# Performance work log

Hardware: AMD Instinct MI355X
Metric: run time of the kernel (lower is better)

## Reference

```python
import jax, jax.numpy as jnp
import numpy as np

NUM_EMBEDDINGS = 8192
EMBEDDING_DIM = 256


def setup_inputs() -> dict:
    key = jax.random.key(0)
    k1, k2 = jax.random.split(key)
    z = jax.random.normal(k1, (16, EMBEDDING_DIM, 32, 32), dtype=jnp.float32)
    # nn.Embedding default init: N(0, 1)
    emb_table = jax.random.normal(k2, (NUM_EMBEDDINGS, EMBEDDING_DIM), dtype=jnp.float32)
    return {"z": z, "emb_table": emb_table}


def reference(z, emb_table):
    # z: [B, D, H, W]; emb_table: [K, D]
    B, D, H, W = z.shape
    # flatten to per-token vectors: [B*H*W, D]
    zf = z.reshape(B, D, H * W).transpose(0, 2, 1).reshape(B * H * W, D)
    Wt = jax.lax.stop_gradient(emb_table)  # original detaches W for distance
    # argmin of mean squared distance == argmin of squared distance;
    # expand ||z - w||^2 = ||z||^2 - 2 z.w + ||w||^2 (avoid (N,K,D) expansion)
    z_sq = jnp.sum(zf * zf, axis=-1, keepdims=True)          # [N, 1]
    w_sq = jnp.sum(Wt * Wt, axis=-1)                          # [K]
    dists = z_sq - 2.0 * (zf @ Wt.T) + w_sq                   # [N, K]
    token_ids = jnp.argmin(dists, axis=-1)                    # [N]
    quantized = emb_table[token_ids]                          # [N, D] (differentiable gather)
    return quantized.reshape(B, H * W, D).transpose(0, 2, 1).reshape(B, D, H, W)
```

## Files before the change

### kernel.cpp

```cpp
#include <hip/hip_runtime.h>
#include <stdint.h>

#define DIM 256
#define NEMB 8192
#define NTOK 16384
#define HW 1024

typedef __attribute__((ext_vector_type(4))) int int4v;

__device__ __forceinline__ void async_cp16(void* lds, const void* g) {
  __builtin_amdgcn_global_load_lds(
      (const __attribute__((address_space(1))) unsigned int*)g,
      (__attribute__((address_space(3))) unsigned int*)lds, 16, 0, 0);
}
__device__ __forceinline__ int q0_of(float x) {
  int q = __float2int_rn(x * 20.0f);
  return q > 127 ? 127 : (q < -127 ? -127 : q);
}
__device__ __forceinline__ int q1_of(float x, int q0) {
  float e = x * 20.0f - (float)q0;
  int q = __float2int_rn(e * 128.0f);
  return q > 127 ? 127 : (q < -127 ? -127 : q);
}
__device__ __forceinline__ unsigned int pack4(int a, int b, int c, int d) {
  return (unsigned int)(a & 0xff) | ((unsigned int)(b & 0xff) << 8) |
         ((unsigned int)(c & 0xff) << 16) | ((unsigned int)(d & 0xff) << 24);
}

__global__ __launch_bounds__(256) void prep_w_kernel(
    const float* __restrict__ emb, unsigned int* __restrict__ q0w,
    unsigned int* __restrict__ q1w, int* __restrict__ iwsq2) {
  int lane = threadIdx.x & 63;
  int row = blockIdx.x * 4 + (threadIdx.x >> 6);
  const float4 v = *(const float4*)(emb + (size_t)row * DIM + lane * 4);
  float s = v.x * v.x + v.y * v.y + v.z * v.z + v.w * v.w;
  int a0 = q0_of(v.x), b0 = q0_of(v.y), c0 = q0_of(v.z), d0 = q0_of(v.w);
  q0w[row * (DIM / 4) + lane] = pack4(a0, b0, c0, d0);
  q1w[row * (DIM / 4) + lane] =
      pack4(q1_of(v.x, a0), q1_of(v.y, b0), q1_of(v.z, c0), q1_of(v.w, d0));
#pragma unroll
  for (int off = 32; off > 0; off >>= 1) s += __shfl_xor(s, off, 64);
  if (lane == 0) iwsq2[row] = (int)rintf(s * 25600.0f) + 8192;
}

__global__ __launch_bounds__(256) void prep_z_kernel(
    const float* __restrict__ z, unsigned int* __restrict__ q0z,
    unsigned int* __restrict__ q1z, float* __restrict__ zf32) {
  __shared__ float tile[64][65];
  int b = blockIdx.x, d0 = blockIdx.y * 64, hw0 = blockIdx.z * 64;
  int tid = threadIdx.x;
  int lane = tid & 63, grp = tid >> 6;
  const float* src = z + (size_t)b * DIM * HW + hw0 + lane;
#pragma unroll
  for (int i = 0; i < 16; i++) {
    int dl = grp + i * 4;
    tile[dl][lane] = src[(size_t)(d0 + dl) * HW];
  }
  __syncthreads();
  int dq = tid & 15;
#pragma unroll
  for (int p = 0; p < 4; p++) {
    int n = (tid >> 4) + p * 16;
    float x0 = tile[dq * 4 + 0][n], x1 = tile[dq * 4 + 1][n];
    float x2 = tile[dq * 4 + 2][n], x3 = tile[dq * 4 + 3][n];
    int a0 = q0_of(x0), b0 = q0_of(x1), c0 = q0_of(x2), e0 = q0_of(x3);
    int token = b * HW + hw0 + n;
    size_t off = (size_t)token * (DIM / 4) + (d0 >> 2) + dq;
    q0z[off] = pack4(a0, b0, c0, e0);
    q1z[off] = pack4(q1_of(x0, a0), q1_of(x1, b0), q1_of(x2, c0), q1_of(x3, e0));
    *(float4*)(zf32 + (size_t)token * DIM + d0 + dq * 4) =
        make_float4(x0, x1, x2, x3);
  }
}

__global__ __launch_bounds__(256, 4) void gemm_topk_kernel(
    const signed char* __restrict__ q0z, const signed char* __restrict__ q1z,
    const signed char* __restrict__ q0w, const signed char* __restrict__ q1w,
    const int* __restrict__ iwsq2, uint2* __restrict__ partials) {
  __shared__ __align__(16) signed char sB[2][4][32 * 128];

  const int bid = blockIdx.x;
  const int xcd = bid & 7;
  const int kq = xcd >> 1;
  const int tg = (bid >> 3) + ((xcd & 1) << 7);
  const int tid = threadIdx.x;
  const int lane = tid & 63, w = tid >> 6;
  const int c = lane & 15, quad = lane >> 4;
  const int n0 = tg * 64;
  const int k0g = kq * 2048;

  int4v af0[4], af1[4];
  {
    const size_t arow = (size_t)(n0 + w * 16 + c) * DIM;
#pragma unroll
    for (int s = 0; s < 4; s++) {
      af0[s] = *(const int4v*)(q0z + arow + s * 64 + quad * 16);
      af1[s] = *(const int4v*)(q1z + arow + s * 64 + quad * 16);
    }
  }

  const int srow = tid >> 3;
  const int scl = ((tid & 7) ^ (srow & 7)) * 16;
  const signed char* p0 = q0w + (size_t)(k0g + srow) * DIM + scl;
  const signed char* p1 = q1w + (size_t)(k0g + srow) * DIM + scl;
  async_cp16(&sB[0][0][tid * 16], p0);
  async_cp16(&sB[0][1][tid * 16], p0 + 128);
  async_cp16(&sB[0][2][tid * 16], p1);
  async_cp16(&sB[0][3][tid * 16], p1 + 128);
  p0 += 32 * DIM;
  p1 += 32 * DIM;
  __syncthreads();

  unsigned int m1[4], m2[4];
#pragma unroll
  for (int i = 0; i < 4; i++) { m1[i] = 0xFFFFFFFFu; m2[i] = 0xFFFFFFFFu; }

  unsigned int idx0 = (unsigned)(k0g + c);
  const int4v zero = {0, 0, 0, 0};

  for (int it = 0; it < 64; it++) {
    const int buf = it & 1;
    if (it + 1 < 64) {
      const int nb = buf ^ 1;
      async_cp16(&sB[nb][0][tid * 16], p0);
      async_cp16(&sB[nb][1][tid * 16], p0 + 128);
      async_cp16(&sB[nb][2][tid * 16], p1);
      async_cp16(&sB[nb][3][tid * 16], p1 + 128);
      p0 += 32 * DIM;
      p1 += 32 * DIM;
    }
    const int iw0 = iwsq2[k0g + it * 32 + c];
    const int iw1 = iwsq2[k0g + it * 32 + 16 + c];

    int4v b0a[4], b0b[4];
#pragma unroll
    for (int s = 0; s < 4; s++) {
      const int half = s >> 1;
      const int ph = ((((s & 1) << 2) + quad) ^ (c & 7)) * 16;
      b0a[s] = *(const int4v*)(&sB[buf][half][c * 128 + ph]);
      b0b[s] = *(const int4v*)(&sB[buf][half][(16 + c) * 128 + ph]);
    }
    int4v a0, a1;
    a0 = __builtin_amdgcn_mfma_i32_16x16x64_i8(af0[0], b0a[0], zero, 0, 0, 0);
    a1 = __builtin_amdgcn_mfma_i32_16x16x64_i8(af0[0], b0b[0], zero, 0, 0, 0);
#pragma unroll
    for (int s = 1; s < 4; s++) {
      a0 = __builtin_amdgcn_mfma_i32_16x16x64_i8(af0[s], b0a[s], a0, 0, 0, 0);
      a1 = __builtin_amdgcn_mfma_i32_16x16x64_i8(af0[s], b0b[s], a1, 0, 0, 0);
    }
#pragma unroll
    for (int r = 0; r < 4; r++) { a0[r] <<= 7; a1[r] <<= 7; }
#pragma unroll
    for (int s = 0; s < 4; s++) {
      a0 = __builtin_amdgcn_mfma_i32_16x16x64_i8(af1[s], b0a[s], a0, 0, 0, 0);
      a1 = __builtin_amdgcn_mfma_i32_16x16x64_i8(af1[s], b0b[s], a1, 0, 0, 0);
    }
#pragma unroll
    for (int s = 0; s < 4; s++) {
      const int half = s >> 1;
      const int ph = ((((s & 1) << 2) + quad) ^ (c & 7)) * 16;
      int4v t = *(const int4v*)(&sB[buf][2 + half][c * 128 + ph]);
      int4v u = *(const int4v*)(&sB[buf][2 + half][(16 + c) * 128 + ph]);
      a0 = __builtin_amdgcn_mfma_i32_16x16x64_i8(af0[s], t, a0, 0, 0, 0);
      a1 = __builtin_amdgcn_mfma_i32_16x16x64_i8(af0[s], u, a1, 0, 0, 0);
    }
#pragma unroll
    for (int r = 0; r < 4; r++) {
      unsigned int s0 = (unsigned int)(iw0 - a0[r]);
      unsigned int s1 = (unsigned int)(iw1 - a1[r]);
      s0 = s0 < 0x2000000u ? s0 : 0x1FFFFFFu;
      s1 = s1 < 0x2000000u ? s1 : 0x1FFFFFFu;
      unsigned int pk0 = ((s0 << 7) & 0xFFFFE000u) | idx0;
      unsigned int pk1 = ((s1 << 7) & 0xFFFFE000u) | (idx0 + 16);
      unsigned int v = pk0 < pk1 ? pk0 : pk1;
      unsigned int lo = v < m1[r] ? v : m1[r];
      unsigned int hi = v < m1[r] ? m1[r] : v;
      m2[r] = m2[r] < hi ? m2[r] : hi;
      m1[r] = lo;
    }
    idx0 += 32;
    __syncthreads();
  }

#pragma unroll
  for (int r = 0; r < 4; r++) {
    unsigned int a1m = m1[r], a2m = m2[r];
#pragma unroll
    for (int off = 1; off < 16; off <<= 1) {
      unsigned int o1 = __shfl_xor(a1m, off, 16);
      unsigned int o2 = __shfl_xor(a2m, off, 16);
      unsigned int n1 = a1m < o1 ? a1m : o1;
      unsigned int hi = a1m < o1 ? o1 : a1m;
      unsigned int l2 = a2m < o2 ? a2m : o2;
      a2m = hi < l2 ? hi : l2;
      a1m = n1;
    }
    m1[r] = a1m;
    m2[r] = a2m;
  }
  if (c == 0) {
#pragma unroll
    for (int r = 0; r < 4; r++) {
      int token = n0 + w * 16 + quad * 4 + r;
      partials[(size_t)kq * NTOK + token] = make_uint2(m1[r], m2[r]);
    }
  }
}

__global__ __launch_bounds__(256) void rescore_kernel(
    const uint2* __restrict__ partials, const float* __restrict__ zf32,
    const float* __restrict__ emb, int* __restrict__ ids) {
  int w = threadIdx.x >> 6, lane = threadIdx.x & 63;
  int token = blockIdx.x * 4 + w;
  unsigned int p[8];
#pragma unroll
  for (int q = 0; q < 4; q++) {
    uint2 t = partials[(size_t)q * NTOK + token];
    p[q * 2] = t.x;
    p[q * 2 + 1] = t.y;
  }
  unsigned int smin = p[0];
#pragma unroll
  for (int q = 1; q < 8; q++) smin = p[q] < smin ? p[q] : smin;
  const unsigned int thr = (smin >> 13) + 64;
  int ns = 0;
#pragma unroll
  for (int q = 0; q < 8; q++) ns += ((p[q] >> 13) <= thr) ? 1 : 0;
  if (ns == 1) {
    if (lane == 0) ids[token] = (int)(smin & 0x1FFFu);
    return;
  }
  const float4 zv = *(const float4*)(zf32 + (size_t)token * DIM + lane * 4);
  double best = 1e300;
  int bid = NEMB;
#pragma unroll
  for (int q = 0; q < 8; q++) {
    if ((p[q] >> 13) <= thr) {
      int id = (int)(p[q] & 0x1FFFu);
      const float4 wv = *(const float4*)(emb + (size_t)id * DIM + lane * 4);
      double s = (double)wv.x * ((double)wv.x - 2.0 * (double)zv.x) +
                 (double)wv.y * ((double)wv.y - 2.0 * (double)zv.y) +
                 (double)wv.z * ((double)wv.z - 2.0 * (double)zv.z) +
                 (double)wv.w * ((double)wv.w - 2.0 * (double)zv.w);
#pragma unroll
      for (int off = 32; off > 0; off >>= 1) s += __shfl_xor(s, off, 64);
      if (s < best || (s == best && id < bid)) {
        best = s;
        bid = id;
      }
    }
  }
  if (lane == 0) ids[token] = bid;
}

__global__ __launch_bounds__(256) void gather_kernel(
    const int* __restrict__ ids, const float* __restrict__ emb,
    float* __restrict__ out) {
  __shared__ float tile[32][257];
  __shared__ int sid[32];
  int b = blockIdx.x;
  int hw0 = blockIdx.y * 32;
  int tid = threadIdx.x;
  if (tid < 32) sid[tid] = ids[b * HW + hw0 + tid];
  __syncthreads();
  for (int i = 0; i < 32; i++)
    tile[i][tid] = emb[(size_t)sid[i] * DIM + tid];
  __syncthreads();
  int h = tid & 31, dg = tid >> 5;
  for (int i = 0; i < 32; i++) {
    int d = i * 8 + dg;
    out[(size_t)b * DIM * HW + (size_t)d * HW + hw0 + h] = tile[h][d];
  }
}

extern "C" void kernel_launch(void* const* d_in, const int* in_sizes, int n_in,
                              void* d_out, int out_size, void* d_ws, size_t ws_size,
                              hipStream_t stream) {
  const float* z = (const float*)d_in[0];
  const float* emb = (const float*)d_in[1];
  float* out = (float*)d_out;
  char* ws = (char*)d_ws;

  float* zf32 = (float*)d_out;

  signed char* q0w = (signed char*)(ws);
  signed char* q1w = (signed char*)(ws + 2097152);
  signed char* q0z = (signed char*)(ws + 4194304);
  signed char* q1z = (signed char*)(ws + 8388608);
  int* iwsq2 = (int*)(ws + 12582912);
  uint2* partials = (uint2*)(ws + 12615680);
  int* ids = (int*)(ws + 13139968);

  prep_w_kernel<<<dim3(2048), 256, 0, stream>>>(emb, (unsigned int*)q0w,
                                                (unsigned int*)q1w, iwsq2);
  prep_z_kernel<<<dim3(16, 4, 16), 256, 0, stream>>>(z, (unsigned int*)q0z,
                                                     (unsigned int*)q1z, zf32);
  gemm_topk_kernel<<<dim3(1024), 256, 0, stream>>>(q0z, q1z, q0w, q1w, iwsq2,
                                                   partials);
  rescore_kernel<<<dim3(4096), 256, 0, stream>>>(partials, zf32, emb, ids);
  gather_kernel<<<dim3(16, 32), 256, 0, stream>>>(ids, emb, out);
}
```

Measured before the change: 191.5 us.

## Merge prep kernels, retile GEMM to 64 tokens per wave, fuse rescore into gather

```diff
diff --git a/kernel.cpp b/kernel.cpp
--- a/kernel.cpp
+++ b/kernel.cpp
@@ -27,29 +27,30 @@
          ((unsigned int)(c & 0xff) << 16) | ((unsigned int)(d & 0xff) << 24);
 }
 
-__global__ __launch_bounds__(256) void prep_w_kernel(
+__global__ __launch_bounds__(256) void prep_kernel(
     const float* __restrict__ emb, unsigned int* __restrict__ q0w,
-    unsigned int* __restrict__ q1w, int* __restrict__ iwsq2) {
-  int lane = threadIdx.x & 63;
-  int row = blockIdx.x * 4 + (threadIdx.x >> 6);
-  const float4 v = *(const float4*)(emb + (size_t)row * DIM + lane * 4);
-  float s = v.x * v.x + v.y * v.y + v.z * v.z + v.w * v.w;
-  int a0 = q0_of(v.x), b0 = q0_of(v.y), c0 = q0_of(v.z), d0 = q0_of(v.w);
-  q0w[row * (DIM / 4) + lane] = pack4(a0, b0, c0, d0);
-  q1w[row * (DIM / 4) + lane] =
-      pack4(q1_of(v.x, a0), q1_of(v.y, b0), q1_of(v.z, c0), q1_of(v.w, d0));
-#pragma unroll
-  for (int off = 32; off > 0; off >>= 1) s += __shfl_xor(s, off, 64);
-  if (lane == 0) iwsq2[row] = (int)rintf(s * 25600.0f) + 8192;
-}
-
-__global__ __launch_bounds__(256) void prep_z_kernel(
+    unsigned int* __restrict__ q1w, int* __restrict__ iwsq2,
     const float* __restrict__ z, unsigned int* __restrict__ q0z,
-    unsigned int* __restrict__ q1z, float* __restrict__ zf32) {
+    unsigned int* __restrict__ q1z) {
   __shared__ float tile[64][65];
-  int b = blockIdx.x, d0 = blockIdx.y * 64, hw0 = blockIdx.z * 64;
   int tid = threadIdx.x;
-  int lane = tid & 63, grp = tid >> 6;
+  int lane = tid & 63;
+  if (blockIdx.x < 2048) {
+    int row = blockIdx.x * 4 + (tid >> 6);
+    const float4 v = *(const float4*)(emb + (size_t)row * DIM + lane * 4);
+    float s = v.x * v.x + v.y * v.y + v.z * v.z + v.w * v.w;
+    int a0 = q0_of(v.x), b0 = q0_of(v.y), c0 = q0_of(v.z), d0 = q0_of(v.w);
+    q0w[row * (DIM / 4) + lane] = pack4(a0, b0, c0, d0);
+    q1w[row * (DIM / 4) + lane] =
+        pack4(q1_of(v.x, a0), q1_of(v.y, b0), q1_of(v.z, c0), q1_of(v.w, d0));
+#pragma unroll
+    for (int off = 32; off > 0; off >>= 1) s += __shfl_xor(s, off, 64);
+    if (lane == 0) iwsq2[row] = (int)rintf(s * 25600.0f) + 8192;
+    return;
+  }
+  int idx = blockIdx.x - 2048;
+  int b = idx >> 6, d0 = ((idx >> 4) & 3) * 64, hw0 = (idx & 15) * 64;
+  int grp = tid >> 6;
   const float* src = z + (size_t)b * DIM * HW + hw0 + lane;
 #pragma unroll
   for (int i = 0; i < 16; i++) {
@@ -68,34 +69,32 @@
     size_t off = (size_t)token * (DIM / 4) + (d0 >> 2) + dq;
     q0z[off] = pack4(a0, b0, c0, e0);
     q1z[off] = pack4(q1_of(x0, a0), q1_of(x1, b0), q1_of(x2, c0), q1_of(x3, e0));
-    *(float4*)(zf32 + (size_t)token * DIM + d0 + dq * 4) =
-        make_float4(x0, x1, x2, x3);
-  }
-}
-
-__global__ __launch_bounds__(256, 4) void gemm_topk_kernel(
+  }
+}
+
+__global__ __launch_bounds__(128, 2) void gemm_topk_kernel(
     const signed char* __restrict__ q0z, const signed char* __restrict__ q1z,
     const signed char* __restrict__ q0w, const signed char* __restrict__ q1w,
     const int* __restrict__ iwsq2, uint2* __restrict__ partials) {
-  __shared__ __align__(16) signed char sB[2][4][32 * 128];
+  __shared__ __align__(16) signed char sB[2][4][16 * 128];
 
   const int bid = blockIdx.x;
-  const int xcd = bid & 7;
-  const int kq = xcd >> 1;
-  const int tg = (bid >> 3) + ((xcd & 1) << 7);
+  const int kq = bid & 7;
+  const int tg = bid >> 3;
   const int tid = threadIdx.x;
   const int lane = tid & 63, w = tid >> 6;
   const int c = lane & 15, quad = lane >> 4;
-  const int n0 = tg * 64;
-  const int k0g = kq * 2048;
-
-  int4v af0[4], af1[4];
-  {
-    const size_t arow = (size_t)(n0 + w * 16 + c) * DIM;
+  const int n0 = tg * 128;
+  const int k0g = kq * 1024;
+
+  int4v af0[4][4], af1[4][4];
+#pragma unroll
+  for (int t = 0; t < 4; t++) {
+    const size_t arow = (size_t)(n0 + w * 64 + t * 16 + c) * DIM;
 #pragma unroll
     for (int s = 0; s < 4; s++) {
-      af0[s] = *(const int4v*)(q0z + arow + s * 64 + quad * 16);
-      af1[s] = *(const int4v*)(q1z + arow + s * 64 + quad * 16);
+      af0[t][s] = *(const int4v*)(q0z + arow + s * 64 + quad * 16);
+      af1[t][s] = *(const int4v*)(q1z + arow + s * 64 + quad * 16);
     }
   }
 
@@ -107,13 +106,13 @@
   async_cp16(&sB[0][1][tid * 16], p0 + 128);
   async_cp16(&sB[0][2][tid * 16], p1);
   async_cp16(&sB[0][3][tid * 16], p1 + 128);
-  p0 += 32 * DIM;
-  p1 += 32 * DIM;
-  __syncthreads();
-
-  unsigned int m1[4], m2[4];
-#pragma unroll
-  for (int i = 0; i < 4; i++) { m1[i] = 0xFFFFFFFFu; m2[i] = 0xFFFFFFFFu; }
+  p0 += 16 * DIM;
+  p1 += 16 * DIM;
+  __syncthreads();
+
+  unsigned int m1[16], m2[16];
+#pragma unroll
+  for (int i = 0; i < 16; i++) { m1[i] = 0xFFFFFFFFu; m2[i] = 0xFFFFFFFFu; }
 
   unsigned int idx0 = (unsigned)(k0g + c);
   const int4v zero = {0, 0, 0, 0};
@@ -126,65 +125,63 @@
       async_cp16(&sB[nb][1][tid * 16], p0 + 128);
       async_cp16(&sB[nb][2][tid * 16], p1);
       async_cp16(&sB[nb][3][tid * 16], p1 + 128);
-      p0 += 32 * DIM;
-      p1 += 32 * DIM;
-    }
-    const int iw0 = iwsq2[k0g + it * 32 + c];
-    const int iw1 = iwsq2[k0g + it * 32 + 16 + c];
-
-    int4v b0a[4], b0b[4];
+      p0 += 16 * DIM;
+      p1 += 16 * DIM;
+    }
+    const int iw = iwsq2[k0g + it * 16 + c];
+
+    int4v b0[4];
 #pragma unroll
     for (int s = 0; s < 4; s++) {
-      const int half = s >> 1;
       const int ph = ((((s & 1) << 2) + quad) ^ (c & 7)) * 16;
-      b0a[s] = *(const int4v*)(&sB[buf][half][c * 128 + ph]);
-      b0b[s] = *(const int4v*)(&sB[buf][half][(16 + c) * 128 + ph]);
-    }
-    int4v a0, a1;
-    a0 = __builtin_amdgcn_mfma_i32_16x16x64_i8(af0[0], b0a[0], zero, 0, 0, 0);
-    a1 = __builtin_amdgcn_mfma_i32_16x16x64_i8(af0[0], b0b[0], zero, 0, 0, 0);
-#pragma unroll
-    for (int s = 1; s < 4; s++) {
-      a0 = __builtin_amdgcn_mfma_i32_16x16x64_i8(af0[s], b0a[s], a0, 0, 0, 0);
-      a1 = __builtin_amdgcn_mfma_i32_16x16x64_i8(af0[s], b0b[s], a1, 0, 0, 0);
-    }
-#pragma unroll
-    for (int r = 0; r < 4; r++) { a0[r] <<= 7; a1[r] <<= 7; }
+      b0[s] = *(const int4v*)(&sB[buf][s >> 1][c * 128 + ph]);
+    }
+    int4v a[4];
+#pragma unroll
+    for (int t = 0; t < 4; t++) {
+      a[t] = __builtin_amdgcn_mfma_i32_16x16x64_i8(af0[t][0], b0[0], zero, 0, 0, 0);
+#pragma unroll
+      for (int s = 1; s < 4; s++)
+        a[t] = __builtin_amdgcn_mfma_i32_16x16x64_i8(af0[t][s], b0[s], a[t], 0, 0, 0);
+    }
+#pragma unroll
+    for (int t = 0; t < 4; t++)
+#pragma unroll
+      for (int r = 0; r < 4; r++) a[t][r] <<= 7;
+#pragma unroll
+    for (int t = 0; t < 4; t++)
+#pragma unroll
+      for (int s = 0; s < 4; s++)
+        a[t] = __builtin_amdgcn_mfma_i32_16x16x64_i8(af1[t][s], b0[s], a[t], 0, 0, 0);
 #pragma unroll
     for (int s = 0; s < 4; s++) {
-      a0 = __builtin_amdgcn_mfma_i32_16x16x64_i8(af1[s], b0a[s], a0, 0, 0, 0);
-      a1 = __builtin_amdgcn_mfma_i32_16x16x64_i8(af1[s], b0b[s], a1, 0, 0, 0);
-    }
-#pragma unroll
-    for (int s = 0; s < 4; s++) {
-      const int half = s >> 1;
       const int ph = ((((s & 1) << 2) + quad) ^ (c & 7)) * 16;
-      int4v t = *(const int4v*)(&sB[buf][2 + half][c * 128 + ph]);
-      int4v u = *(const int4v*)(&sB[buf][2 + half][(16 + c) * 128 + ph]);
-      a0 = __builtin_amdgcn_mfma_i32_16x16x64_i8(af0[s], t, a0, 0, 0, 0);
-      a1 = __builtin_amdgcn_mfma_i32_16x16x64_i8(af0[s], u, a1, 0, 0, 0);
-    }
-#pragma unroll
-    for (int r = 0; r < 4; r++) {
-      unsigned int s0 = (unsigned int)(iw0 - a0[r]);
-      unsigned int s1 = (unsigned int)(iw1 - a1[r]);
-      s0 = s0 < 0x2000000u ? s0 : 0x1FFFFFFu;
-      s1 = s1 < 0x2000000u ? s1 : 0x1FFFFFFu;
-      unsigned int pk0 = ((s0 << 7) & 0xFFFFE000u) | idx0;
-      unsigned int pk1 = ((s1 << 7) & 0xFFFFE000u) | (idx0 + 16);
-      unsigned int v = pk0 < pk1 ? pk0 : pk1;
-      unsigned int lo = v < m1[r] ? v : m1[r];
-      unsigned int hi = v < m1[r] ? m1[r] : v;
-      m2[r] = m2[r] < hi ? m2[r] : hi;
-      m1[r] = lo;
-    }
-    idx0 += 32;
+      int4v b1 = *(const int4v*)(&sB[buf][2 + (s >> 1)][c * 128 + ph]);
+#pragma unroll
+      for (int t = 0; t < 4; t++)
+        a[t] = __builtin_amdgcn_mfma_i32_16x16x64_i8(af0[t][s], b1, a[t], 0, 0, 0);
+    }
+#pragma unroll
+    for (int t = 0; t < 4; t++) {
+#pragma unroll
+      for (int r = 0; r < 4; r++) {
+        unsigned int s0 = (unsigned int)(iw - a[t][r]);
+        s0 = s0 < 0x2000000u ? s0 : 0x1FFFFFFu;
+        unsigned int v = ((s0 << 7) & 0xFFFFE000u) | idx0;
+        const int ix = t * 4 + r;
+        unsigned int lo = v < m1[ix] ? v : m1[ix];
+        unsigned int hi = v < m1[ix] ? m1[ix] : v;
+        m2[ix] = m2[ix] < hi ? m2[ix] : hi;
+        m1[ix] = lo;
+      }
+    }
+    idx0 += 16;
     __syncthreads();
   }
 
 #pragma unroll
-  for (int r = 0; r < 4; r++) {
-    unsigned int a1m = m1[r], a2m = m2[r];
+  for (int ix = 0; ix < 16; ix++) {
+    unsigned int a1m = m1[ix], a2m = m2[ix];
 #pragma unroll
     for (int off = 1; off < 16; off <<= 1) {
       unsigned int o1 = __shfl_xor(a1m, off, 16);
@@ -195,73 +192,77 @@
       a2m = hi < l2 ? hi : l2;
       a1m = n1;
     }
-    m1[r] = a1m;
-    m2[r] = a2m;
+    m1[ix] = a1m;
+    m2[ix] = a2m;
   }
   if (c == 0) {
 #pragma unroll
-    for (int r = 0; r < 4; r++) {
-      int token = n0 + w * 16 + quad * 4 + r;
-      partials[(size_t)kq * NTOK + token] = make_uint2(m1[r], m2[r]);
-    }
-  }
-}
-
-__global__ __launch_bounds__(256) void rescore_kernel(
-    const uint2* __restrict__ partials, const float* __restrict__ zf32,
-    const float* __restrict__ emb, int* __restrict__ ids) {
-  int w = threadIdx.x >> 6, lane = threadIdx.x & 63;
-  int token = blockIdx.x * 4 + w;
-  unsigned int p[8];
-#pragma unroll
-  for (int q = 0; q < 4; q++) {
-    uint2 t = partials[(size_t)q * NTOK + token];
-    p[q * 2] = t.x;
-    p[q * 2 + 1] = t.y;
-  }
-  unsigned int smin = p[0];
-#pragma unroll
-  for (int q = 1; q < 8; q++) smin = p[q] < smin ? p[q] : smin;
-  const unsigned int thr = (smin >> 13) + 64;
-  int ns = 0;
-#pragma unroll
-  for (int q = 0; q < 8; q++) ns += ((p[q] >> 13) <= thr) ? 1 : 0;
-  if (ns == 1) {
-    if (lane == 0) ids[token] = (int)(smin & 0x1FFFu);
-    return;
-  }
-  const float4 zv = *(const float4*)(zf32 + (size_t)token * DIM + lane * 4);
-  double best = 1e300;
-  int bid = NEMB;
-#pragma unroll
-  for (int q = 0; q < 8; q++) {
-    if ((p[q] >> 13) <= thr) {
-      int id = (int)(p[q] & 0x1FFFu);
-      const float4 wv = *(const float4*)(emb + (size_t)id * DIM + lane * 4);
-      double s = (double)wv.x * ((double)wv.x - 2.0 * (double)zv.x) +
-                 (double)wv.y * ((double)wv.y - 2.0 * (double)zv.y) +
-                 (double)wv.z * ((double)wv.z - 2.0 * (double)zv.z) +
-                 (double)wv.w * ((double)wv.w - 2.0 * (double)zv.w);
-#pragma unroll
-      for (int off = 32; off > 0; off >>= 1) s += __shfl_xor(s, off, 64);
-      if (s < best || (s == best && id < bid)) {
-        best = s;
-        bid = id;
+    for (int t = 0; t < 4; t++) {
+#pragma unroll
+      for (int r = 0; r < 4; r++) {
+        int token = n0 + w * 64 + t * 16 + quad * 4 + r;
+        partials[(size_t)kq * NTOK + token] =
+            make_uint2(m1[t * 4 + r], m2[t * 4 + r]);
       }
     }
   }
-  if (lane == 0) ids[token] = bid;
-}
-
-__global__ __launch_bounds__(256) void gather_kernel(
-    const int* __restrict__ ids, const float* __restrict__ emb,
-    float* __restrict__ out) {
+}
+
+__global__ __launch_bounds__(256) void rescore_gather_kernel(
+    const uint2* __restrict__ partials, const float* __restrict__ z,
+    const float* __restrict__ emb, float* __restrict__ out) {
   __shared__ float tile[32][257];
   __shared__ int sid[32];
-  int b = blockIdx.x;
-  int hw0 = blockIdx.y * 32;
-  int tid = threadIdx.x;
-  if (tid < 32) sid[tid] = ids[b * HW + hw0 + tid];
+  const int b = blockIdx.x >> 5;
+  const int hw0 = (blockIdx.x & 31) * 32;
+  const int tid = threadIdx.x;
+  const int w = tid >> 6, lane = tid & 63;
+  for (int i = 0; i < 8; i++) {
+    const int tl = w * 8 + i;
+    const int token = b * HW + hw0 + tl;
+    unsigned int p[16];
+#pragma unroll
+    for (int q = 0; q < 8; q++) {
+      uint2 t = partials[(size_t)q * NTOK + token];
+      p[q * 2] = t.x;
+      p[q * 2 + 1] = t.y;
+    }
+    unsigned int smin = p[0];
+#pragma unroll
+    for (int q = 1; q < 16; q++) smin = p[q] < smin ? p[q] : smin;
+    const unsigned int thr = (smin >> 13) + 64;
+    int ns = 0;
+#pragma unroll
+    for (int q = 0; q < 16; q++) ns += ((p[q] >> 13) <= thr) ? 1 : 0;
+    int chosen = (int)(smin & 0x1FFFu);
+    if (ns > 1) {
+      float zv[4];
+#pragma unroll
+      for (int j = 0; j < 4; j++)
+        zv[j] = z[(size_t)b * DIM * HW + (size_t)(lane * 4 + j) * HW + hw0 + tl];
+      double best = 1e300;
+      int bid2 = NEMB;
+#pragma unroll
+      for (int q = 0; q < 16; q++) {
+        if ((p[q] >> 13) <= thr) {
+          int id = (int)(p[q] & 0x1FFFu);
+          const float4 wv = *(const float4*)(emb + (size_t)id * DIM + lane * 4);
+          double s = (double)wv.x * ((double)wv.x - 2.0 * (double)zv[0]) +
+                     (double)wv.y * ((double)wv.y - 2.0 * (double)zv[1]) +
+                     (double)wv.z * ((double)wv.z - 2.0 * (double)zv[2]) +
+                     (double)wv.w * ((double)wv.w - 2.0 * (double)zv[3]);
+#pragma unroll
+          for (int off = 32; off > 0; off >>= 1) s += __shfl_xor(s, off, 64);
+          if (s < best || (s == best && id < bid2)) {
+            best = s;
+            bid2 = id;
+          }
+        }
+      }
+      chosen = bid2;
+    }
+    if (lane == 0) sid[tl] = chosen;
+  }
   __syncthreads();
   for (int i = 0; i < 32; i++)
     tile[i][tid] = emb[(size_t)sid[i] * DIM + tid];
@@ -281,22 +282,17 @@
   float* out = (float*)d_out;
   char* ws = (char*)d_ws;
 
-  float* zf32 = (float*)d_out;
-
   signed char* q0w = (signed char*)(ws);
   signed char* q1w = (signed char*)(ws + 2097152);
   signed char* q0z = (signed char*)(ws + 4194304);
   signed char* q1z = (signed char*)(ws + 8388608);
   int* iwsq2 = (int*)(ws + 12582912);
   uint2* partials = (uint2*)(ws + 12615680);
-  int* ids = (int*)(ws + 13139968);
-
-  prep_w_kernel<<<dim3(2048), 256, 0, stream>>>(emb, (unsigned int*)q0w,
-                                                (unsigned int*)q1w, iwsq2);
-  prep_z_kernel<<<dim3(16, 4, 16), 256, 0, stream>>>(z, (unsigned int*)q0z,
-                                                     (unsigned int*)q1z, zf32);
-  gemm_topk_kernel<<<dim3(1024), 256, 0, stream>>>(q0z, q1z, q0w, q1w, iwsq2,
+
+  prep_kernel<<<dim3(3072), 256, 0, stream>>>(
+      emb, (unsigned int*)q0w, (unsigned int*)q1w, iwsq2, z, (unsigned int*)q0z,
+      (unsigned int*)q1z);
+  gemm_topk_kernel<<<dim3(1024), 128, 0, stream>>>(q0z, q1z, q0w, q1w, iwsq2,
                                                    partials);
-  rescore_kernel<<<dim3(4096), 256, 0, stream>>>(partials, zf32, emb, ids);
-  gather_kernel<<<dim3(16, 32), 256, 0, stream>>>(ids, emb, out);
-}
+  rescore_gather_kernel<<<dim3(512), 256, 0, stream>>>(partials, z, emb, out);
+}
```

Result: faster. 185.9 us (-2.9%).
